# Optimization experiments

Hardware: AMD Instinct MI355X
Metric: run time of the kernel (lower is better)

Reference implementation:

```python
import jax, jax.numpy as jnp
import numpy as np

N = 16384        # nodes
E = 262144       # edges (avg degree 16)
MUL = 64         # multiplicity per irrep
RDIM = 8         # radial embedding dim
NEURONS = 64     # radial MLP hidden width
NSPECIES = 4
AVG_NEIGH = 16.0
SQRT3 = 1.7320508075688772


def setup_inputs() -> dict:
    key = jax.random.key(0)
    k = jax.random.split(key, 16)
    ey1 = jax.random.normal(k[3], (E, 3), jnp.float32)
    ey1 = ey1 / jnp.linalg.norm(ey1, axis=-1, keepdims=True)  # l=1 spherical harmonics ~ unit edge vectors
    return {
        'node_x0': jax.random.normal(k[0], (N, MUL), jnp.float32),
        'node_x1': jax.random.normal(k[1], (N, MUL, 3), jnp.float32),
        'edge_y0': jnp.ones((E,), jnp.float32),            # l=0 SH is constant
        'edge_y1': ey1,
        'radial_embedding': jax.random.uniform(k[4], (E, RDIM), jnp.float32),
        'senders': jax.random.randint(k[5], (E,), 0, N, dtype=jnp.int32),
        'receivers': jax.random.randint(k[6], (E,), 0, N, dtype=jnp.int32),
        'node_species': jax.random.randint(k[7], (N,), 0, NSPECIES, dtype=jnp.int32),
        'Wup0': jax.random.normal(k[8], (MUL, MUL), jnp.float32),
        'Wup1': jax.random.normal(k[9], (MUL, MUL), jnp.float32),
        'Rw1': jax.random.normal(k[10], (RDIM, NEURONS), jnp.float32),
        'Rw2': jax.random.normal(k[11], (NEURONS, 4 * MUL), jnp.float32),
        'Wd0': jax.random.normal(k[12], (2 * MUL, 2 * MUL), jnp.float32),
        'Wd1': jax.random.normal(k[13], (2 * MUL, MUL), jnp.float32),
        'Wsc0': jax.random.normal(k[14], (NSPECIES, MUL, 2 * MUL), jnp.float32),
        'Wsc1': jax.random.normal(k[15], (NSPECIES, MUL, MUL), jnp.float32),
    }


def reference(node_x0, node_x1, edge_y0, edge_y1, radial_embedding,
              senders, receivers, node_species,
              Wup0, Wup1, Rw1, Rw2, Wd0, Wd1, Wsc0, Wsc1):
    inv = 1.0 / jnp.sqrt(jnp.float32(MUL))
    # ---- linear_up: per-irrep channel mixing --------------------------------
    h0 = (node_x0 @ Wup0) * inv                              # [N, MUL] 0e
    h1 = jnp.einsum('nmc,mk->nkc', node_x1, Wup1) * inv      # [N, MUL, 3] 1o
    # ---- radial MLP -> per-edge tensor-product path weights -----------------
    hid = jax.nn.silu((radial_embedding @ Rw1) / jnp.sqrt(jnp.float32(RDIM)))
    w = ((hid @ Rw2) / jnp.sqrt(jnp.float32(NEURONS))).reshape(E, 4, MUL)
    # ---- gather sender features ---------------------------------------------
    s0 = h0[senders]                                         # [E, MUL]
    s1 = h1[senders]                                         # [E, MUL, 3]
    # ---- CG tensor product (lmax=1) with radial weights ----------------------
    m0a = w[:, 0] * s0 * edge_y0[:, None]                    # 0e x 0e -> 0e
    m0b = w[:, 1] * jnp.einsum('emc,ec->em', s1, edge_y1) / SQRT3  # 1o . 1o -> 0e
    m1a = w[:, 2][:, :, None] * s0[:, :, None] * edge_y1[:, None, :]  # 0e x 1o -> 1o
    m1b = w[:, 3][:, :, None] * s1 * edge_y0[:, None, None]          # 1o x 0e -> 1o
    # ---- scatter-sum to receivers, normalize by sqrt(avg_num_neighbours) ----
    denom = jnp.sqrt(jnp.float32(AVG_NEIGH))
    a0 = jax.ops.segment_sum(jnp.concatenate([m0a, m0b], axis=-1), receivers, num_segments=N) / denom  # [N, 2*MUL]
    a1 = jax.ops.segment_sum(jnp.concatenate([m1a, m1b], axis=1), receivers, num_segments=N) / denom   # [N, 2*MUL, 3]
    # ---- linear_down to gate irreps (MUL scalars + MUL gates, MUL vectors) ---
    inv2 = 1.0 / jnp.sqrt(jnp.float32(2 * MUL))
    d0 = (a0 @ Wd0) * inv2                                   # [N, 2*MUL]
    d1 = jnp.einsum('nmc,mk->nkc', a1, Wd1) * inv2           # [N, MUL, 3]
    # ---- species-indexed self connection (gather weights by species) --------
    all0 = jnp.einsum('nm,smk->nsk', node_x0, Wsc0) * inv    # [N, S, 2*MUL]
    sc0 = jnp.take_along_axis(all0, node_species[:, None, None], axis=1)[:, 0]
    all1 = jnp.einsum('nmc,smk->nskc', node_x1, Wsc1) * inv  # [N, S, MUL, 3]
    sc1 = jnp.take_along_axis(all1, node_species[:, None, None, None], axis=1)[:, 0]
    f0 = 0.5 * (d0 + sc0)
    f1 = 0.5 * (d1 + sc1)
    # ---- equivariant gate: even_act on scalars, even_gate_act on gates ------
    scalars = jax.nn.silu(f0[:, :MUL])                       # [N, MUL]
    gates = jax.nn.silu(f0[:, MUL:])                         # [N, MUL]
    vectors = f1 * gates[:, :, None]                         # [N, MUL, 3]
    return scalars, vectors
```

## Files before the change

kernel.cpp:

```cpp
#include <hip/hip_runtime.h>

#define NN 16384
#define NE 262144
#define N64 (NN * 64)

typedef unsigned short u16;
typedef __attribute__((ext_vector_type(8))) short short8;
typedef __attribute__((ext_vector_type(4))) float f32x4;

__device__ __forceinline__ float us2f(u16 u) {
    union { unsigned int i; float f; } v; v.i = ((unsigned int)u) << 16; return v.f;
}
__device__ __forceinline__ u16 f2us(float x) {
    union { float f; unsigned int i; } u; u.f = x;
    unsigned int r = u.i + 0x7FFF + ((u.i >> 16) & 1);
    return (u16)(r >> 16);
}
__device__ __forceinline__ float silu_f(float x) { return x / (1.0f + __expf(-x)); }
__device__ __forceinline__ float ldf(const void* p, long i, int f) {
    return f ? ((const float*)p)[i] : us2f(((const u16*)p)[i]);
}
__device__ __forceinline__ short8 f32x8_to_bf16(const float* p) {
    f32x4 a = *reinterpret_cast<const f32x4*>(p);
    f32x4 b = *reinterpret_cast<const f32x4*>(p + 4);
    short8 r;
    r[0] = (short)f2us(a[0]); r[1] = (short)f2us(a[1]);
    r[2] = (short)f2us(a[2]); r[3] = (short)f2us(a[3]);
    r[4] = (short)f2us(b[0]); r[5] = (short)f2us(b[1]);
    r[6] = (short)f2us(b[2]); r[7] = (short)f2us(b[3]);
    return r;
}

__global__ void k_sniff(const u16* __restrict__ re, int* __restrict__ flag) {
    int t = threadIdx.x;
    int hit = (re[t] >= 0x4000) ? 1 : 0;
    unsigned long long b = __ballot(hit);
    if (t == 0) *flag = (__popcll(b) >= 4) ? 1 : 0;
}

#define SB0 1048576L
#define SB1 4194304L
#define SB2 4456448L
#define SB3 5242880L
#define SB4 7340032L
#define SB5 7344128L
#define SB6 7348224L
#define SB7 7348736L
#define SB8 7365120L
#define SB9 7381504L
#define SB10 7389696L
#define SB11 7422464L
#define SB12 7438848L

__global__ void k_convert(const void* x0, const void* x1, const void* ey0, const void* ey1,
                          const void* re, const void* Wup0, const void* Wup1, const void* Rw1,
                          const void* Rw2, const void* Wd0, const void* Wd1, const void* Wsc0,
                          const void* Wsc1, const int* __restrict__ flag,
                          const int* __restrict__ recv, int* __restrict__ cnt,
                          u16* c_x0, u16* x1T, u16* c_ey0, u16* c_ey1, u16* c_re,
                          u16* c_Wup0, u16* c_Wup1, u16* c_Rw1, u16* c_Rw2,
                          u16* c_Wd0, u16* c_Wd1, u16* c_Wsc0, u16* c_Wsc1) {
    long i = (long)blockIdx.x * 256 + threadIdx.x;
    int f = *flag;
    if (i < NE) atomicAdd(&cnt[recv[i]], 1);
    if (i < SB0)       { c_x0[i]          = f2us(ldf(x0, i, f)); }
    else if (i < SB1)  {
        long j = i - SB0;
        int n = (int)(j / 192); int r = (int)(j % 192); int m = r / 3; int c = r % 3;
        x1T[(long)c * N64 + (long)n * 64 + m] = f2us(ldf(x1, j, f));
    }
    else if (i < SB2)  { c_ey0[i - SB1]   = f2us(ldf(ey0, i - SB1, f)); }
    else if (i < SB3)  { c_ey1[i - SB2]   = f2us(ldf(ey1, i - SB2, f)); }
    else if (i < SB4)  { c_re[i - SB3]    = f2us(ldf(re, i - SB3, f)); }
    else if (i < SB5)  { long j = i - SB4;  long r = j >> 6, c = j & 63;
                         c_Wup0[c * 64 + r]  = f2us(ldf(Wup0, j, f)); }
    else if (i < SB6)  { long j = i - SB5;  long r = j >> 6, c = j & 63;
                         c_Wup1[c * 64 + r]  = f2us(ldf(Wup1, j, f)); }
    else if (i < SB7)  { c_Rw1[i - SB6]   = f2us(ldf(Rw1, i - SB6, f)); }
    else if (i < SB8)  { long j = i - SB7;  long r = j >> 8, c = j & 255;
                         c_Rw2[c * 64 + r]   = f2us(ldf(Rw2, j, f)); }
    else if (i < SB9)  { long j = i - SB8;  long r = j >> 7, c = j & 127;
                         c_Wd0[c * 128 + r]  = f2us(ldf(Wd0, j, f)); }
    else if (i < SB10) { long j = i - SB9;  long r = j >> 6, c = j & 63;
                         c_Wd1[c * 128 + r]  = f2us(ldf(Wd1, j, f)); }
    else if (i < SB11) { long j = i - SB10; long s = j >> 13, rm = j & 8191;
                         long r = rm >> 7, c = rm & 127;
                         c_Wsc0[s * 8192 + c * 64 + r] = f2us(ldf(Wsc0, j, f)); }
    else               { long j = i - SB11; long s = j >> 12, rm = j & 4095;
                         long r = rm >> 6, c = rm & 63;
                         c_Wsc1[s * 4096 + c * 64 + r] = f2us(ldf(Wsc1, j, f)); }
}

__global__ void k_scan(const int* __restrict__ cnt, int* __restrict__ offs,
                       int* __restrict__ cursor) {
    __shared__ int sd[256];
    int t = threadIdx.x;
    int base = t * 64;
    const int4* c4 = (const int4*)cnt;
    int loc[64];
#pragma unroll
    for (int i = 0; i < 16; i++) {
        int4 v = c4[t * 16 + i];
        loc[i * 4 + 0] = v.x; loc[i * 4 + 1] = v.y; loc[i * 4 + 2] = v.z; loc[i * 4 + 3] = v.w;
    }
    int sum = 0;
#pragma unroll
    for (int i = 0; i < 64; i++) sum += loc[i];
    sd[t] = sum; __syncthreads();
    for (int off = 1; off < 256; off <<= 1) {
        int v = (t >= off) ? sd[t - off] : 0;
        __syncthreads();
        sd[t] += v;
        __syncthreads();
    }
    int run = sd[t] - sum;
    for (int i = 0; i < 64; i++) {
        offs[base + i] = run; cursor[base + i] = run;
        run += loc[i];
    }
    if (t == 255) offs[NN] = run;
}

__global__ void k_scatter(const int* __restrict__ recv, const int* __restrict__ senders,
                          const u16* __restrict__ ey0, const u16* __restrict__ ey1,
                          int* __restrict__ cursor, int4* __restrict__ meta) {
    int e = blockIdx.x * 256 + threadIdx.x;
    int node = recv[e];
    int p = atomicAdd(&cursor[node], 1);
    unsigned y0  = ey0[e];
    unsigned y1x = ey1[(long)e * 3 + 0];
    unsigned y1y = ey1[(long)e * 3 + 1];
    unsigned y1z = ey1[(long)e * 3 + 2];
    int4 m;
    m.x = senders[e];
    m.y = (int)(y0 | (y1x << 16));
    m.z = (int)(y1y | (y1z << 16));
    m.w = (int)((unsigned)e | ((unsigned)node << 18));
    meta[p] = m;
}

__global__ void k_up_gemm(const u16* __restrict__ x0, const u16* __restrict__ x1T,
                          const u16* __restrict__ Wup0, const u16* __restrict__ Wup1,
                          u16* __restrict__ h) {
    int inst = blockIdx.y;
    int wv = threadIdx.x >> 6, lane = threadIdx.x & 63;
    int lhi = lane >> 4, llo = lane & 15;
    int mb = blockIdx.x * 256 + wv * 64;
    const u16* B = (inst == 0) ? Wup0 : Wup1;
    const u16* A = (inst == 0) ? x0 : (x1T + (long)(inst - 1) * N64);

    short8 bfr[4][2];
#pragma unroll
    for (int t = 0; t < 4; t++)
#pragma unroll
        for (int s = 0; s < 2; s++)
            bfr[t][s] = *reinterpret_cast<const short8*>(B + (long)(t * 16 + llo) * 64 + s * 32 + lhi * 8);

    f32x4 acc[4][4];
#pragma unroll
    for (int i = 0; i < 4; i++)
#pragma unroll
        for (int t = 0; t < 4; t++) acc[i][t] = 0.0f;

#pragma unroll
    for (int s = 0; s < 2; s++) {
        short8 af[4];
#pragma unroll
        for (int i = 0; i < 4; i++)
            af[i] = *reinterpret_cast<const short8*>(A + (long)(mb + i * 16 + llo) * 64 + s * 32 + lhi * 8);
#pragma unroll
        for (int i = 0; i < 4; i++)
#pragma unroll
            for (int t = 0; t < 4; t++)
                acc[i][t] = __builtin_amdgcn_mfma_f32_16x16x32_bf16(af[i], bfr[t][s], acc[i][t], 0, 0, 0);
    }
#pragma unroll
    for (int i = 0; i < 4; i++)
#pragma unroll
        for (int t = 0; t < 4; t++)
#pragma unroll
            for (int r = 0; r < 4; r++)
                h[(long)(mb + i * 16 + lhi * 4 + r) * 256 + (t * 16 + llo) * 4 + inst] =
                    f2us(acc[i][t][r] * 0.125f);
}

#define RROW 276
__global__ void __launch_bounds__(256, 3)
k_edge(const u16* __restrict__ re, const u16* __restrict__ Rw1,
       const u16* __restrict__ Rw2, const int4* __restrict__ meta,
       const u16* __restrict__ h, float* __restrict__ abuf32) {
    __shared__ u16 hid_s[64][72];
    __shared__ u16 w_lds[64 * RROW];
    int tid = threadIdx.x;
    int wv = tid >> 6, lane = tid & 63, lhi = lane >> 4, llo = lane & 15;
    int p0 = blockIdx.x * 64;

    {
        int el = tid >> 2;
        int jb = (tid & 3) * 16;
        int e = ((const int*)meta)[(long)(p0 + el) * 4 + 3] & 0x3FFFF;
        short8 r8 = *reinterpret_cast<const short8*>(re + (long)e * 8);
        float rr[8];
#pragma unroll
        for (int r = 0; r < 8; r++) rr[r] = us2f((u16)r8[r]);
        float hv[16];
#pragma unroll
        for (int q = 0; q < 2; q++) {
            short8 w8 = *reinterpret_cast<const short8*>(Rw1 + jb + q * 8);
#pragma unroll
            for (int j = 0; j < 8; j++) hv[q * 8 + j] = rr[0] * us2f((u16)w8[j]);
        }
#pragma unroll
        for (int r = 1; r < 8; r++) {
#pragma unroll
            for (int q = 0; q < 2; q++) {
                short8 w8 = *reinterpret_cast<const short8*>(Rw1 + (long)r * 64 + jb + q * 8);
#pragma unroll
                for (int j = 0; j < 8; j++) hv[q * 8 + j] += rr[r] * us2f((u16)w8[j]);
            }
        }
#pragma unroll
        for (int q = 0; q < 4; q++) {
            ushort4 pk;
            pk.x = f2us(silu_f(hv[q * 4 + 0] * 0.35355339059327373f));
            pk.y = f2us(silu_f(hv[q * 4 + 1] * 0.35355339059327373f));
            pk.z = f2us(silu_f(hv[q * 4 + 2] * 0.35355339059327373f));
            pk.w = f2us(silu_f(hv[q * 4 + 3] * 0.35355339059327373f));
            *reinterpret_cast<ushort4*>(&hid_s[el][jb + q * 4]) = pk;
        }
    }
    __syncthreads();

    {
        short8 bfr[4][2];
#pragma unroll
        for (int t = 0; t < 4; t++)
#pragma unroll
            for (int s = 0; s < 2; s++)
                bfr[t][s] = *reinterpret_cast<const short8*>(
                    Rw2 + (long)(wv * 64 + t * 16 + llo) * 64 + s * 32 + lhi * 8);
        f32x4 acc[4][4];
#pragma unroll
        for (int i = 0; i < 4; i++)
#pragma unroll
            for (int t = 0; t < 4; t++) acc[i][t] = 0.0f;
#pragma unroll
        for (int s = 0; s < 2; s++) {
            short8 af[4];
#pragma unroll
            for (int i = 0; i < 4; i++)
                af[i] = *reinterpret_cast<const short8*>(&hid_s[i * 16 + llo][s * 32 + lhi * 8]);
#pragma unroll
            for (int i = 0; i < 4; i++)
#pragma unroll
                for (int t = 0; t < 4; t++)
                    acc[i][t] = __builtin_amdgcn_mfma_f32_16x16x32_bf16(af[i], bfr[t][s], acc[i][t], 0, 0, 0);
        }
#pragma unroll
        for (int i = 0; i < 4; i++)
#pragma unroll
            for (int t = 0; t < 4; t++)
#pragma unroll
                for (int r = 0; r < 4; r++)
                    w_lds[(i * 16 + lhi * 4 + r) * RROW + wv * 64 + t * 16 + llo] =
                        f2us(acc[i][t][r] * 0.125f);
    }
    __syncthreads();

    {
        const float qn = 0.25f;
        const float rs3 = 0.57735026918962576f;
        int l = lane;
        int base = wv * 16;
        float acc[8];
#pragma unroll
        for (int r = 0; r < 8; r++) acc[r] = 0.f;
        int cur = -1;

        int4 m = meta[p0 + base];
        ushort4 hv = *reinterpret_cast<const ushort4*>(h + (long)m.x * 256 + l * 4);

        for (int ss = 0; ss < 16; ss++) {
            int4 mn = m; ushort4 hn = hv;
            if (ss + 1 < 16) {
                mn = meta[p0 + base + ss + 1];
                hn = *reinterpret_cast<const ushort4*>(h + (long)mn.x * 256 + l * 4);
            }
            int node = (int)(((unsigned)m.w) >> 18);
            if (node != cur) {
                if (cur >= 0) {
                    float* dst = abuf32 + (long)cur * 512 + l;
                    atomicAdd(dst,        acc[0] * qn);
                    atomicAdd(dst + 64,   acc[1] * qn * rs3);
                    atomicAdd(dst + 128,  acc[2] * qn);
                    atomicAdd(dst + 192,  acc[3] * qn);
                    atomicAdd(dst + 256,  acc[4] * qn);
                    atomicAdd(dst + 320,  acc[5] * qn);
                    atomicAdd(dst + 384,  acc[6] * qn);
                    atomicAdd(dst + 448,  acc[7] * qn);
                }
                cur = node;
#pragma unroll
                for (int r = 0; r < 8; r++) acc[r] = 0.f;
            }
            int sl = base + ss;
            float w0 = us2f(w_lds[sl * RROW + l]);
            float w1 = us2f(w_lds[sl * RROW + 64 + l]);
            float w2 = us2f(w_lds[sl * RROW + 128 + l]);
            float w3 = us2f(w_lds[sl * RROW + 192 + l]);
            float y0  = us2f((u16)((unsigned)m.y & 0xffff));
            float y1x = us2f((u16)((unsigned)m.y >> 16));
            float y1y = us2f((u16)((unsigned)m.z & 0xffff));
            float y1z = us2f((u16)((unsigned)m.z >> 16));
            float s0 = us2f(hv.x), s1x = us2f(hv.y), s1y = us2f(hv.z), s1z = us2f(hv.w);
            acc[0] += w0 * s0 * y0;
            acc[1] += w1 * (s1x * y1x + s1y * y1y + s1z * y1z);
            acc[2] += w2 * s0 * y1x;  acc[3] += w3 * s1x * y0;
            acc[4] += w2 * s0 * y1y;  acc[5] += w3 * s1y * y0;
            acc[6] += w2 * s0 * y1z;  acc[7] += w3 * s1z * y0;
            m = mn; hv = hn;
        }
        {
            float* dst = abuf32 + (long)cur * 512 + l;
            atomicAdd(dst,        acc[0] * qn);
            atomicAdd(dst + 64,   acc[1] * qn * rs3);
            atomicAdd(dst + 128,  acc[2] * qn);
            atomicAdd(dst + 192,  acc[3] * qn);
            atomicAdd(dst + 256,  acc[4] * qn);
            atomicAdd(dst + 320,  acc[5] * qn);
            atomicAdd(dst + 384,  acc[6] * qn);
            atomicAdd(dst + 448,  acc[7] * qn);
        }
    }
}

#define DN 32
__global__ void __launch_bounds__(320, 3)
k_down(const float* __restrict__ abuf32, const u16* __restrict__ x0,
       const u16* __restrict__ x1T, const int* __restrict__ species,
       const u16* __restrict__ Wd0T, const u16* __restrict__ Wd1T,
       const u16* __restrict__ Wsc0T, const u16* __restrict__ Wsc1T,
       float* __restrict__ out) {
    __shared__ float gate_s[DN][65];
    __shared__ float vec_s[DN * 192];
    __shared__ int sp_s[DN];
    int tid = threadIdx.x;
    int g = tid >> 6;
    int lane = tid & 63, lhi = lane >> 4, llo = lane & 15;
    int node0 = blockIdx.x * DN;
    if (tid < DN) sp_s[tid] = species[node0 + tid];
    __syncthreads();

    const float* Ad; const u16* BdT; int bcol;
    const u16* As; const u16* BsT; int sstr;
    if (g <= 1) { Ad = abuf32; BdT = Wd0T; bcol = g * 64; As = x0; BsT = Wsc0T; sstr = 8192; }
    else        { Ad = abuf32 + (g - 1) * 128; BdT = Wd1T; bcol = 0;
                  As = x1T + (long)(g - 2) * N64; BsT = Wsc1T; sstr = 4096; }

    const float inv2 = 0.08838834764831845f;
    const float inv  = 0.125f;

    short8 a2[DN / 16][2];
#pragma unroll
    for (int rt = 0; rt < DN / 16; rt++)
#pragma unroll
        for (int ks = 0; ks < 2; ks++)
            a2[rt][ks] = *reinterpret_cast<const short8*>(
                As + (long)(node0 + rt * 16 + llo) * 64 + ks * 32 + lhi * 8);

    f32x4 res[DN / 16][4];
#pragma unroll
    for (int rt = 0; rt < DN / 16; rt++)
#pragma unroll
        for (int ct = 0; ct < 4; ct++) res[rt][ct] = 0.0f;

    for (int s = 0; s < 4; s++) {
        short8 bs[4][2];
#pragma unroll
        for (int ct = 0; ct < 4; ct++)
#pragma unroll
            for (int ks = 0; ks < 2; ks++)
                bs[ct][ks] = *reinterpret_cast<const short8*>(
                    BsT + (long)s * sstr + (long)(bcol + ct * 16 + llo) * 64 + ks * 32 + lhi * 8);
#pragma unroll
        for (int rt = 0; rt < DN / 16; rt++) {
            f32x4 accs[4];
#pragma unroll
            for (int ct = 0; ct < 4; ct++) accs[ct] = 0.0f;
#pragma unroll
            for (int ks = 0; ks < 2; ks++)
#pragma unroll
                for (int ct = 0; ct < 4; ct++)
                    accs[ct] = __builtin_amdgcn_mfma_f32_16x16x32_bf16(a2[rt][ks], bs[ct][ks], accs[ct], 0, 0, 0);
#pragma unroll
            for (int r = 0; r < 4; r++) {
                int sp = sp_s[rt * 16 + lhi * 4 + r];
                if (sp == s)
#pragma unroll
                    for (int ct = 0; ct < 4; ct++) res[rt][ct][r] = accs[ct][r];
            }
        }
    }

    short8 bd[4][4];
#pragma unroll
    for (int ct = 0; ct < 4; ct++)
#pragma unroll
        for (int ks = 0; ks < 4; ks++)
            bd[ct][ks] = *reinterpret_cast<const short8*>(
                BdT + (long)(bcol + ct * 16 + llo) * 128 + ks * 32 + lhi * 8);

#pragma unroll
    for (int rt = 0; rt < DN / 16; rt++) {
        f32x4 accd[4];
#pragma unroll
        for (int ct = 0; ct < 4; ct++) accd[ct] = 0.0f;
#pragma unroll
        for (int ks = 0; ks < 4; ks++) {
            short8 a = f32x8_to_bf16(Ad + (long)(node0 + rt * 16 + llo) * 512 + ks * 32 + lhi * 8);
#pragma unroll
            for (int ct = 0; ct < 4; ct++)
                accd[ct] = __builtin_amdgcn_mfma_f32_16x16x32_bf16(a, bd[ct][ks], accd[ct], 0, 0, 0);
        }
#pragma unroll
        for (int ct = 0; ct < 4; ct++)
#pragma unroll
            for (int r = 0; r < 4; r++) {
                float fvv = 0.5f * (accd[ct][r] * inv2 + res[rt][ct][r] * inv);
                int row = rt * 16 + lhi * 4 + r;
                int col = ct * 16 + llo;
                if (g == 0) {
                    out[(long)(node0 + row) * 64 + col] = silu_f(fvv);
                } else if (g == 1) {
                    gate_s[row][col] = silu_f(fvv);
                } else {
                    vec_s[row * 192 + col * 3 + (g - 2)] = fvv;
                }
            }
    }
    __syncthreads();

    {
        float* vout = out + (long)N64 + (long)node0 * 192;
        for (int q4 = tid; q4 < DN * 48; q4 += 320) {
            int q = q4 * 4;
            int row = q4 / 48;
            int rem = q - row * 192;
            f32x4 v = *reinterpret_cast<const f32x4*>(&vec_s[q]);
#pragma unroll
            for (int e = 0; e < 4; e++) v[e] *= gate_s[row][(rem + e) / 3];
            *reinterpret_cast<f32x4*>(vout + q) = v;
        }
    }
}

extern "C" void kernel_launch(void* const* d_in, const int* in_sizes, int n_in,
                              void* d_out, int out_size, void* d_ws, size_t ws_size,
                              hipStream_t stream) {
    const int* senders   = (const int*)d_in[5];
    const int* receivers = (const int*)d_in[6];
    const int* species   = (const int*)d_in[7];
    float* out = (float*)d_out;

    char* ws = (char*)d_ws;
    size_t o = 0;
    auto alloc = [&](size_t bytes) { size_t p = o; o = (o + bytes + 255) & ~255UL; return p; };
    int* flag   = (int*)(ws + alloc(4));
    int* cnt    = (int*)(ws + alloc((size_t)NN * 4));
    int* offs   = (int*)(ws + alloc((size_t)(NN + 1) * 4));
    int* cursor = (int*)(ws + alloc((size_t)NN * 4));
    int4* meta  = (int4*)(ws + alloc((size_t)NE * 16));
    u16* c_x0   = (u16*)(ws + alloc(SB0 * 2));
    u16* x1T    = (u16*)(ws + alloc((size_t)3 * N64 * 2));
    u16* c_ey0  = (u16*)(ws + alloc((SB2 - SB1) * 2));
    u16* c_ey1  = (u16*)(ws + alloc((SB3 - SB2) * 2));
    u16* c_re   = (u16*)(ws + alloc((SB4 - SB3) * 2));
    u16* c_Wup0 = (u16*)(ws + alloc((SB5 - SB4) * 2));
    u16* c_Wup1 = (u16*)(ws + alloc((SB6 - SB5) * 2));
    u16* c_Rw1  = (u16*)(ws + alloc((SB7 - SB6) * 2));
    u16* c_Rw2  = (u16*)(ws + alloc((SB8 - SB7) * 2));
    u16* c_Wd0  = (u16*)(ws + alloc((SB9 - SB8) * 2));
    u16* c_Wd1  = (u16*)(ws + alloc((SB10 - SB9) * 2));
    u16* c_Wsc0 = (u16*)(ws + alloc((SB11 - SB10) * 2));
    u16* c_Wsc1 = (u16*)(ws + alloc((SB12 - SB11) * 2));
    u16* h      = (u16*)(ws + alloc((size_t)NN * 256 * 2));
    float* abuf32 = (float*)(ws + alloc((size_t)NN * 512 * 4));

    k_sniff<<<1, 64, 0, stream>>>((const u16*)d_in[4], flag);
    (void)hipMemsetAsync(cnt, 0, (size_t)NN * 4, stream);
    (void)hipMemsetAsync(abuf32, 0, (size_t)NN * 512 * 4, stream);
    k_convert<<<29058, 256, 0, stream>>>(d_in[0], d_in[1], d_in[2], d_in[3], d_in[4],
        d_in[8], d_in[9], d_in[10], d_in[11], d_in[12], d_in[13], d_in[14], d_in[15],
        flag, receivers, cnt,
        c_x0, x1T, c_ey0, c_ey1, c_re,
        c_Wup0, c_Wup1, c_Rw1, c_Rw2, c_Wd0, c_Wd1, c_Wsc0, c_Wsc1);
    k_scan<<<1, 256, 0, stream>>>(cnt, offs, cursor);
    k_scatter<<<NE / 256, 256, 0, stream>>>(receivers, senders, c_ey0, c_ey1,
                                            cursor, meta);

    k_up_gemm<<<dim3(NN / 256, 4), 256, 0, stream>>>(c_x0, x1T, c_Wup0, c_Wup1, h);

    k_edge<<<NE / 64, 256, 0, stream>>>(c_re, c_Rw1, c_Rw2, meta, h, abuf32);

    k_down<<<NN / DN, 320, 0, stream>>>(abuf32, c_x0, x1T, species,
                                        c_Wd0, c_Wd1, c_Wsc0, c_Wsc1, out);
}
```

Baseline: 276.1 us.

## Replace global atomics with plain stores and LDS merge for receiver segments in edge kernel

Using the CSR offsets, the edge kernel now writes node aggregates with plain stores when a receiver's whole edge segment lies inside one wave's slice of the block. Segments that span waves inside the block are merged in LDS with shared atomics, then written once. Only segments crossing block boundaries still use global atomics. The hidden-activation scratch is aliased into the weight LDS buffer, with an added barrier, and occupancy is raised from 3 to 4 blocks per CU. In exchange it adds extra offset loads and branching per flush.

```diff
diff --git a/kernel.cpp b/kernel.cpp
--- a/kernel.cpp
+++ b/kernel.cpp
@@ -184,16 +184,24 @@
                     f2us(acc[i][t][r] * 0.125f);
 }
 
-#define RROW 276
-__global__ void __launch_bounds__(256, 3)
+#define RROW 268
+__global__ void __launch_bounds__(256, 4)
 k_edge(const u16* __restrict__ re, const u16* __restrict__ Rw1,
        const u16* __restrict__ Rw2, const int4* __restrict__ meta,
-       const u16* __restrict__ h, float* __restrict__ abuf32) {
-    __shared__ u16 hid_s[64][72];
+       const u16* __restrict__ h, const int* __restrict__ offs,
+       float* __restrict__ abuf32) {
     __shared__ u16 w_lds[64 * RROW];
+    __shared__ float mrg[3][512];
+    __shared__ int mrg_node[3], mrg_used[3], mrg_cont[3];
+    u16 (*hid_s)[72] = reinterpret_cast<u16 (*)[72]>(w_lds);
+
     int tid = threadIdx.x;
     int wv = tid >> 6, lane = tid & 63, lhi = lane >> 4, llo = lane & 15;
     int p0 = blockIdx.x * 64;
+
+#pragma unroll
+    for (int k = tid; k < 3 * 512; k += 256) (&mrg[0][0])[k] = 0.f;
+    if (tid < 3) mrg_used[tid] = 0;
 
     {
         int el = tid >> 2;
@@ -256,6 +264,7 @@
                 for (int t = 0; t < 4; t++)
                     acc[i][t] = __builtin_amdgcn_mfma_f32_16x16x32_bf16(af[i], bfr[t][s], acc[i][t], 0, 0, 0);
         }
+        __syncthreads();
 #pragma unroll
         for (int i = 0; i < 4; i++)
 #pragma unroll
@@ -271,39 +280,63 @@
         const float qn = 0.25f;
         const float rs3 = 0.57735026918962576f;
         int l = lane;
-        int base = wv * 16;
+        int wb = wv * 16;
         float acc[8];
 #pragma unroll
         for (int r = 0; r < 8; r++) acc[r] = 0.f;
         int cur = -1;
 
-        int4 m = meta[p0 + base];
+        int4 m = meta[p0 + wb];
         ushort4 hv = *reinterpret_cast<const ushort4*>(h + (long)m.x * 256 + l * 4);
+
+        auto flush = [&](int n) {
+            int s = offs[n], e = offs[n + 1];
+            int sb = s < p0 ? p0 : s;
+            int se = e > p0 + 64 ? p0 + 64 : e;
+            int w0 = (sb - p0) >> 4, w1 = (se - 1 - p0) >> 4;
+            float v0 = acc[0] * qn, v1 = acc[1] * qn * rs3;
+            float v2 = acc[2] * qn, v3 = acc[3] * qn;
+            float v4 = acc[4] * qn, v5 = acc[5] * qn;
+            float v6 = acc[6] * qn, v7 = acc[7] * qn;
+            if (w0 == w1) {
+                float* dst = abuf32 + (long)n * 512 + l;
+                if (s >= p0 && e <= p0 + 64) {
+                    dst[0]   = v0; dst[64]  = v1; dst[128] = v2; dst[192] = v3;
+                    dst[256] = v4; dst[320] = v5; dst[384] = v6; dst[448] = v7;
+                } else {
+                    atomicAdd(dst,       v0); atomicAdd(dst + 64,  v1);
+                    atomicAdd(dst + 128, v2); atomicAdd(dst + 192, v3);
+                    atomicAdd(dst + 256, v4); atomicAdd(dst + 320, v5);
+                    atomicAdd(dst + 384, v6); atomicAdd(dst + 448, v7);
+                }
+            } else {
+                int j = w0;
+                if (l == 0) {
+                    mrg_node[j] = n; mrg_used[j] = 1;
+                    mrg_cont[j] = (s >= p0 && e <= p0 + 64) ? 1 : 0;
+                }
+                float* md = &mrg[j][l];
+                atomicAdd(md,       v0); atomicAdd(md + 64,  v1);
+                atomicAdd(md + 128, v2); atomicAdd(md + 192, v3);
+                atomicAdd(md + 256, v4); atomicAdd(md + 320, v5);
+                atomicAdd(md + 384, v6); atomicAdd(md + 448, v7);
+            }
+        };
 
         for (int ss = 0; ss < 16; ss++) {
             int4 mn = m; ushort4 hn = hv;
             if (ss + 1 < 16) {
-                mn = meta[p0 + base + ss + 1];
+                mn = meta[p0 + wb + ss + 1];
                 hn = *reinterpret_cast<const ushort4*>(h + (long)mn.x * 256 + l * 4);
             }
             int node = (int)(((unsigned)m.w) >> 18);
             if (node != cur) {
-                if (cur >= 0) {
-                    float* dst = abuf32 + (long)cur * 512 + l;
-                    atomicAdd(dst,        acc[0] * qn);
-                    atomicAdd(dst + 64,   acc[1] * qn * rs3);
-                    atomicAdd(dst + 128,  acc[2] * qn);
-                    atomicAdd(dst + 192,  acc[3] * qn);
-                    atomicAdd(dst + 256,  acc[4] * qn);
-                    atomicAdd(dst + 320,  acc[5] * qn);
-                    atomicAdd(dst + 384,  acc[6] * qn);
-                    atomicAdd(dst + 448,  acc[7] * qn);
-                }
+                if (cur >= 0) flush(cur);
                 cur = node;
 #pragma unroll
                 for (int r = 0; r < 8; r++) acc[r] = 0.f;
             }
-            int sl = base + ss;
+            int sl = wb + ss;
             float w0 = us2f(w_lds[sl * RROW + l]);
             float w1 = us2f(w_lds[sl * RROW + 64 + l]);
             float w2 = us2f(w_lds[sl * RROW + 128 + l]);
@@ -320,16 +353,21 @@
             acc[6] += w2 * s0 * y1z;  acc[7] += w3 * s1z * y0;
             m = mn; hv = hn;
         }
-        {
-            float* dst = abuf32 + (long)cur * 512 + l;
-            atomicAdd(dst,        acc[0] * qn);
-            atomicAdd(dst + 64,   acc[1] * qn * rs3);
-            atomicAdd(dst + 128,  acc[2] * qn);
-            atomicAdd(dst + 192,  acc[3] * qn);
-            atomicAdd(dst + 256,  acc[4] * qn);
-            atomicAdd(dst + 320,  acc[5] * qn);
-            atomicAdd(dst + 384,  acc[6] * qn);
-            atomicAdd(dst + 448,  acc[7] * qn);
+        flush(cur);
+    }
+    __syncthreads();
+
+#pragma unroll
+    for (int j = 0; j < 3; j++) {
+        if (mrg_used[j]) {
+            int n = mrg_node[j];
+            float* dst = abuf32 + (long)n * 512;
+            float a = mrg[j][tid], b = mrg[j][tid + 256];
+            if (mrg_cont[j]) {
+                dst[tid] = a; dst[tid + 256] = b;
+            } else {
+                atomicAdd(dst + tid, a); atomicAdd(dst + tid + 256, b);
+            }
         }
     }
 }
@@ -500,7 +538,7 @@
 
     k_up_gemm<<<dim3(NN / 256, 4), 256, 0, stream>>>(c_x0, x1T, c_Wup0, c_Wup1, h);
 
-    k_edge<<<NE / 64, 256, 0, stream>>>(c_re, c_Rw1, c_Rw2, meta, h, abuf32);
+    k_edge<<<NE / 64, 256, 0, stream>>>(c_re, c_Rw1, c_Rw2, meta, h, offs, abuf32);
 
     k_down<<<NN / DN, 320, 0, stream>>>(abuf32, c_x0, x1T, species,
                                         c_Wd0, c_Wd1, c_Wsc0, c_Wsc1, out);
```

New measurement: 315.2 us. +14.2%, slower.

## Assign receiver-node ranges to edge blocks, replacing float atomics with bf16 stores

Applied to the files above, without the earlier changes.

The edge kernel now gives each block 16 consecutive receiver nodes and walks their CSR-sorted edge range in 64-edge tiles. Each wave owns whole nodes and writes the aggregated result once with plain stores instead of float atomicAdds. The aggregation buffer shrinks from fp32 to bf16 and no longer needs a memset, and the down kernel reads bf16 directly without converting. The risks are load imbalance from variable node degree, a sequential per-node loop with lower parallelism, and reads of meta past the last edge, which the extra 64-entry padding covers.

```diff
diff --git a/kernel.cpp b/kernel.cpp
--- a/kernel.cpp
+++ b/kernel.cpp
@@ -19,16 +19,6 @@
 __device__ __forceinline__ float silu_f(float x) { return x / (1.0f + __expf(-x)); }
 __device__ __forceinline__ float ldf(const void* p, long i, int f) {
     return f ? ((const float*)p)[i] : us2f(((const u16*)p)[i]);
-}
-__device__ __forceinline__ short8 f32x8_to_bf16(const float* p) {
-    f32x4 a = *reinterpret_cast<const f32x4*>(p);
-    f32x4 b = *reinterpret_cast<const f32x4*>(p + 4);
-    short8 r;
-    r[0] = (short)f2us(a[0]); r[1] = (short)f2us(a[1]);
-    r[2] = (short)f2us(a[2]); r[3] = (short)f2us(a[3]);
-    r[4] = (short)f2us(b[0]); r[5] = (short)f2us(b[1]);
-    r[6] = (short)f2us(b[2]); r[7] = (short)f2us(b[3]);
-    return r;
 }
 
 __global__ void k_sniff(const u16* __restrict__ re, int* __restrict__ flag) {
@@ -184,159 +174,169 @@
                     f2us(acc[i][t][r] * 0.125f);
 }
 
+#define EN 16
 #define RROW 276
 __global__ void __launch_bounds__(256, 3)
 k_edge(const u16* __restrict__ re, const u16* __restrict__ Rw1,
        const u16* __restrict__ Rw2, const int4* __restrict__ meta,
-       const u16* __restrict__ h, float* __restrict__ abuf32) {
+       const u16* __restrict__ h, const int* __restrict__ offs,
+       u16* __restrict__ abuf) {
     __shared__ u16 hid_s[64][72];
     __shared__ u16 w_lds[64 * RROW];
+    __shared__ int offs_s[EN + 1];
     int tid = threadIdx.x;
     int wv = tid >> 6, lane = tid & 63, lhi = lane >> 4, llo = lane & 15;
-    int p0 = blockIdx.x * 64;
-
-    {
-        int el = tid >> 2;
-        int jb = (tid & 3) * 16;
-        int e = ((const int*)meta)[(long)(p0 + el) * 4 + 3] & 0x3FFFF;
-        short8 r8 = *reinterpret_cast<const short8*>(re + (long)e * 8);
-        float rr[8];
-#pragma unroll
-        for (int r = 0; r < 8; r++) rr[r] = us2f((u16)r8[r]);
-        float hv[16];
-#pragma unroll
-        for (int q = 0; q < 2; q++) {
-            short8 w8 = *reinterpret_cast<const short8*>(Rw1 + jb + q * 8);
-#pragma unroll
-            for (int j = 0; j < 8; j++) hv[q * 8 + j] = rr[0] * us2f((u16)w8[j]);
+    int n0 = blockIdx.x * EN;
+    if (tid <= EN) offs_s[tid] = offs[n0 + tid];
+    __syncthreads();
+    int s0 = offs_s[0], s1 = offs_s[EN];
+    int T = (s1 - s0 + 63) >> 6;
+
+    const float qn = 0.25f;
+    const float rs3 = 0.57735026918962576f;
+    int ni = wv;
+    float acc[8];
+#pragma unroll
+    for (int r = 0; r < 8; r++) acc[r] = 0.f;
+
+    for (int t = 0; t < T; t++) {
+        int ts = s0 + t * 64;
+        {
+            int el = tid >> 2;
+            int jb = (tid & 3) * 16;
+            int e = ((const int*)meta)[(long)(ts + el) * 4 + 3] & 0x3FFFF;
+            short8 r8 = *reinterpret_cast<const short8*>(re + (long)e * 8);
+            float rr[8];
+#pragma unroll
+            for (int r = 0; r < 8; r++) rr[r] = us2f((u16)r8[r]);
+            float hv[16];
+#pragma unroll
+            for (int q = 0; q < 2; q++) {
+                short8 w8 = *reinterpret_cast<const short8*>(Rw1 + jb + q * 8);
+#pragma unroll
+                for (int j = 0; j < 8; j++) hv[q * 8 + j] = rr[0] * us2f((u16)w8[j]);
+            }
+#pragma unroll
+            for (int r = 1; r < 8; r++) {
+#pragma unroll
+                for (int q = 0; q < 2; q++) {
+                    short8 w8 = *reinterpret_cast<const short8*>(Rw1 + (long)r * 64 + jb + q * 8);
+#pragma unroll
+                    for (int j = 0; j < 8; j++) hv[q * 8 + j] += rr[r] * us2f((u16)w8[j]);
+                }
+            }
+#pragma unroll
+            for (int q = 0; q < 4; q++) {
+                ushort4 pk;
+                pk.x = f2us(silu_f(hv[q * 4 + 0] * 0.35355339059327373f));
+                pk.y = f2us(silu_f(hv[q * 4 + 1] * 0.35355339059327373f));
+                pk.z = f2us(silu_f(hv[q * 4 + 2] * 0.35355339059327373f));
+                pk.w = f2us(silu_f(hv[q * 4 + 3] * 0.35355339059327373f));
+                *reinterpret_cast<ushort4*>(&hid_s[el][jb + q * 4]) = pk;
+            }
         }
-#pragma unroll
-        for (int r = 1; r < 8; r++) {
-#pragma unroll
-            for (int q = 0; q < 2; q++) {
-                short8 w8 = *reinterpret_cast<const short8*>(Rw1 + (long)r * 64 + jb + q * 8);
-#pragma unroll
-                for (int j = 0; j < 8; j++) hv[q * 8 + j] += rr[r] * us2f((u16)w8[j]);
-            }
+        __syncthreads();
+
+        {
+            short8 bfr[4][2];
+#pragma unroll
+            for (int tt = 0; tt < 4; tt++)
+#pragma unroll
+                for (int s = 0; s < 2; s++)
+                    bfr[tt][s] = *reinterpret_cast<const short8*>(
+                        Rw2 + (long)(wv * 64 + tt * 16 + llo) * 64 + s * 32 + lhi * 8);
+            f32x4 ac[4][4];
+#pragma unroll
+            for (int i = 0; i < 4; i++)
+#pragma unroll
+                for (int tt = 0; tt < 4; tt++) ac[i][tt] = 0.0f;
+#pragma unroll
+            for (int s = 0; s < 2; s++) {
+                short8 af[4];
+#pragma unroll
+                for (int i = 0; i < 4; i++)
+                    af[i] = *reinterpret_cast<const short8*>(&hid_s[i * 16 + llo][s * 32 + lhi * 8]);
+#pragma unroll
+                for (int i = 0; i < 4; i++)
+#pragma unroll
+                    for (int tt = 0; tt < 4; tt++)
+                        ac[i][tt] = __builtin_amdgcn_mfma_f32_16x16x32_bf16(af[i], bfr[tt][s], ac[i][tt], 0, 0, 0);
+            }
+#pragma unroll
+            for (int i = 0; i < 4; i++)
+#pragma unroll
+                for (int tt = 0; tt < 4; tt++)
+#pragma unroll
+                    for (int r = 0; r < 4; r++)
+                        w_lds[(i * 16 + lhi * 4 + r) * RROW + wv * 64 + tt * 16 + llo] =
+                            f2us(ac[i][tt][r] * 0.125f);
         }
-#pragma unroll
-        for (int q = 0; q < 4; q++) {
-            ushort4 pk;
-            pk.x = f2us(silu_f(hv[q * 4 + 0] * 0.35355339059327373f));
-            pk.y = f2us(silu_f(hv[q * 4 + 1] * 0.35355339059327373f));
-            pk.z = f2us(silu_f(hv[q * 4 + 2] * 0.35355339059327373f));
-            pk.w = f2us(silu_f(hv[q * 4 + 3] * 0.35355339059327373f));
-            *reinterpret_cast<ushort4*>(&hid_s[el][jb + q * 4]) = pk;
+        __syncthreads();
+
+        {
+            int te = ts + 64;
+            while (ni < EN) {
+                int rs = offs_s[ni], ren = offs_s[ni + 1];
+                if (rs >= te) break;
+                int a = rs > ts ? rs : ts;
+                int b = ren < te ? ren : te;
+                if (a < b) {
+                    int4 m = meta[a];
+                    ushort4 hv = *reinterpret_cast<const ushort4*>(h + (long)m.x * 256 + lane * 4);
+                    for (int p = a; p < b; p++) {
+                        int4 mn = m; ushort4 hn = hv;
+                        if (p + 1 < b) {
+                            mn = meta[p + 1];
+                            hn = *reinterpret_cast<const ushort4*>(h + (long)mn.x * 256 + lane * 4);
+                        }
+                        int sl = p - ts;
+                        float w0 = us2f(w_lds[sl * RROW + lane]);
+                        float w1 = us2f(w_lds[sl * RROW + 64 + lane]);
+                        float w2 = us2f(w_lds[sl * RROW + 128 + lane]);
+                        float w3 = us2f(w_lds[sl * RROW + 192 + lane]);
+                        float y0  = us2f((u16)((unsigned)m.y & 0xffff));
+                        float y1x = us2f((u16)((unsigned)m.y >> 16));
+                        float y1y = us2f((u16)((unsigned)m.z & 0xffff));
+                        float y1z = us2f((u16)((unsigned)m.z >> 16));
+                        float sv0 = us2f(hv.x), s1x = us2f(hv.y), s1y = us2f(hv.z), s1z = us2f(hv.w);
+                        acc[0] += w0 * sv0 * y0;
+                        acc[1] += w1 * (s1x * y1x + s1y * y1y + s1z * y1z);
+                        acc[2] += w2 * sv0 * y1x;  acc[3] += w3 * s1x * y0;
+                        acc[4] += w2 * sv0 * y1y;  acc[5] += w3 * s1y * y0;
+                        acc[6] += w2 * sv0 * y1z;  acc[7] += w3 * s1z * y0;
+                        m = mn; hv = hn;
+                    }
+                }
+                if (ren <= te) {
+                    u16* ab = abuf + (long)(n0 + ni) * 512 + lane;
+                    ab[0]   = f2us(acc[0] * qn);
+                    ab[64]  = f2us(acc[1] * qn * rs3);
+                    ab[128] = f2us(acc[2] * qn);
+                    ab[192] = f2us(acc[3] * qn);
+                    ab[256] = f2us(acc[4] * qn);
+                    ab[320] = f2us(acc[5] * qn);
+                    ab[384] = f2us(acc[6] * qn);
+                    ab[448] = f2us(acc[7] * qn);
+#pragma unroll
+                    for (int r = 0; r < 8; r++) acc[r] = 0.f;
+                    ni += 4;
+                } else break;
+            }
         }
-    }
-    __syncthreads();
-
-    {
-        short8 bfr[4][2];
-#pragma unroll
-        for (int t = 0; t < 4; t++)
-#pragma unroll
-            for (int s = 0; s < 2; s++)
-                bfr[t][s] = *reinterpret_cast<const short8*>(
-                    Rw2 + (long)(wv * 64 + t * 16 + llo) * 64 + s * 32 + lhi * 8);
-        f32x4 acc[4][4];
-#pragma unroll
-        for (int i = 0; i < 4; i++)
-#pragma unroll
-            for (int t = 0; t < 4; t++) acc[i][t] = 0.0f;
-#pragma unroll
-        for (int s = 0; s < 2; s++) {
-            short8 af[4];
-#pragma unroll
-            for (int i = 0; i < 4; i++)
-                af[i] = *reinterpret_cast<const short8*>(&hid_s[i * 16 + llo][s * 32 + lhi * 8]);
-#pragma unroll
-            for (int i = 0; i < 4; i++)
-#pragma unroll
-                for (int t = 0; t < 4; t++)
-                    acc[i][t] = __builtin_amdgcn_mfma_f32_16x16x32_bf16(af[i], bfr[t][s], acc[i][t], 0, 0, 0);
-        }
-#pragma unroll
-        for (int i = 0; i < 4; i++)
-#pragma unroll
-            for (int t = 0; t < 4; t++)
-#pragma unroll
-                for (int r = 0; r < 4; r++)
-                    w_lds[(i * 16 + lhi * 4 + r) * RROW + wv * 64 + t * 16 + llo] =
-                        f2us(acc[i][t][r] * 0.125f);
-    }
-    __syncthreads();
-
-    {
-        const float qn = 0.25f;
-        const float rs3 = 0.57735026918962576f;
-        int l = lane;
-        int base = wv * 16;
-        float acc[8];
-#pragma unroll
-        for (int r = 0; r < 8; r++) acc[r] = 0.f;
-        int cur = -1;
-
-        int4 m = meta[p0 + base];
-        ushort4 hv = *reinterpret_cast<const ushort4*>(h + (long)m.x * 256 + l * 4);
-
-        for (int ss = 0; ss < 16; ss++) {
-            int4 mn = m; ushort4 hn = hv;
-            if (ss + 1 < 16) {
-                mn = meta[p0 + base + ss + 1];
-                hn = *reinterpret_cast<const ushort4*>(h + (long)mn.x * 256 + l * 4);
-            }
-            int node = (int)(((unsigned)m.w) >> 18);
-            if (node != cur) {
-                if (cur >= 0) {
-                    float* dst = abuf32 + (long)cur * 512 + l;
-                    atomicAdd(dst,        acc[0] * qn);
-                    atomicAdd(dst + 64,   acc[1] * qn * rs3);
-                    atomicAdd(dst + 128,  acc[2] * qn);
-                    atomicAdd(dst + 192,  acc[3] * qn);
-                    atomicAdd(dst + 256,  acc[4] * qn);
-                    atomicAdd(dst + 320,  acc[5] * qn);
-                    atomicAdd(dst + 384,  acc[6] * qn);
-                    atomicAdd(dst + 448,  acc[7] * qn);
-                }
-                cur = node;
-#pragma unroll
-                for (int r = 0; r < 8; r++) acc[r] = 0.f;
-            }
-            int sl = base + ss;
-            float w0 = us2f(w_lds[sl * RROW + l]);
-            float w1 = us2f(w_lds[sl * RROW + 64 + l]);
-            float w2 = us2f(w_lds[sl * RROW + 128 + l]);
-            float w3 = us2f(w_lds[sl * RROW + 192 + l]);
-            float y0  = us2f((u16)((unsigned)m.y & 0xffff));
-            float y1x = us2f((u16)((unsigned)m.y >> 16));
-            float y1y = us2f((u16)((unsigned)m.z & 0xffff));
-            float y1z = us2f((u16)((unsigned)m.z >> 16));
-            float s0 = us2f(hv.x), s1x = us2f(hv.y), s1y = us2f(hv.z), s1z = us2f(hv.w);
-            acc[0] += w0 * s0 * y0;
-            acc[1] += w1 * (s1x * y1x + s1y * y1y + s1z * y1z);
-            acc[2] += w2 * s0 * y1x;  acc[3] += w3 * s1x * y0;
-            acc[4] += w2 * s0 * y1y;  acc[5] += w3 * s1y * y0;
-            acc[6] += w2 * s0 * y1z;  acc[7] += w3 * s1z * y0;
-            m = mn; hv = hn;
-        }
-        {
-            float* dst = abuf32 + (long)cur * 512 + l;
-            atomicAdd(dst,        acc[0] * qn);
-            atomicAdd(dst + 64,   acc[1] * qn * rs3);
-            atomicAdd(dst + 128,  acc[2] * qn);
-            atomicAdd(dst + 192,  acc[3] * qn);
-            atomicAdd(dst + 256,  acc[4] * qn);
-            atomicAdd(dst + 320,  acc[5] * qn);
-            atomicAdd(dst + 384,  acc[6] * qn);
-            atomicAdd(dst + 448,  acc[7] * qn);
-        }
+        __syncthreads();
+    }
+    while (ni < EN) {
+        u16* ab = abuf + (long)(n0 + ni) * 512 + lane;
+        u16 z = f2us(0.f);
+        ab[0] = z; ab[64] = z; ab[128] = z; ab[192] = z;
+        ab[256] = z; ab[320] = z; ab[384] = z; ab[448] = z;
+        ni += 4;
     }
 }
 
 #define DN 32
 __global__ void __launch_bounds__(320, 3)
-k_down(const float* __restrict__ abuf32, const u16* __restrict__ x0,
+k_down(const u16* __restrict__ abuf, const u16* __restrict__ x0,
        const u16* __restrict__ x1T, const int* __restrict__ species,
        const u16* __restrict__ Wd0T, const u16* __restrict__ Wd1T,
        const u16* __restrict__ Wsc0T, const u16* __restrict__ Wsc1T,
@@ -351,10 +351,10 @@
     if (tid < DN) sp_s[tid] = species[node0 + tid];
     __syncthreads();
 
-    const float* Ad; const u16* BdT; int bcol;
+    const u16* Ad; const u16* BdT; int bcol;
     const u16* As; const u16* BsT; int sstr;
-    if (g <= 1) { Ad = abuf32; BdT = Wd0T; bcol = g * 64; As = x0; BsT = Wsc0T; sstr = 8192; }
-    else        { Ad = abuf32 + (g - 1) * 128; BdT = Wd1T; bcol = 0;
+    if (g <= 1) { Ad = abuf; BdT = Wd0T; bcol = g * 64; As = x0; BsT = Wsc0T; sstr = 8192; }
+    else        { Ad = abuf + (g - 1) * 128; BdT = Wd1T; bcol = 0;
                   As = x1T + (long)(g - 2) * N64; BsT = Wsc1T; sstr = 4096; }
 
     const float inv2 = 0.08838834764831845f;
@@ -417,7 +417,8 @@
         for (int ct = 0; ct < 4; ct++) accd[ct] = 0.0f;
 #pragma unroll
         for (int ks = 0; ks < 4; ks++) {
-            short8 a = f32x8_to_bf16(Ad + (long)(node0 + rt * 16 + llo) * 512 + ks * 32 + lhi * 8);
+            short8 a = *reinterpret_cast<const short8*>(
+                Ad + (long)(node0 + rt * 16 + llo) * 512 + ks * 32 + lhi * 8);
 #pragma unroll
             for (int ct = 0; ct < 4; ct++)
                 accd[ct] = __builtin_amdgcn_mfma_f32_16x16x32_bf16(a, bd[ct][ks], accd[ct], 0, 0, 0);
@@ -469,7 +470,7 @@
     int* cnt    = (int*)(ws + alloc((size_t)NN * 4));
     int* offs   = (int*)(ws + alloc((size_t)(NN + 1) * 4));
     int* cursor = (int*)(ws + alloc((size_t)NN * 4));
-    int4* meta  = (int4*)(ws + alloc((size_t)NE * 16));
+    int4* meta  = (int4*)(ws + alloc((size_t)(NE + 64) * 16));
     u16* c_x0   = (u16*)(ws + alloc(SB0 * 2));
     u16* x1T    = (u16*)(ws + alloc((size_t)3 * N64 * 2));
     u16* c_ey0  = (u16*)(ws + alloc((SB2 - SB1) * 2));
@@ -484,11 +485,10 @@
     u16* c_Wsc0 = (u16*)(ws + alloc((SB11 - SB10) * 2));
     u16* c_Wsc1 = (u16*)(ws + alloc((SB12 - SB11) * 2));
     u16* h      = (u16*)(ws + alloc((size_t)NN * 256 * 2));
-    float* abuf32 = (float*)(ws + alloc((size_t)NN * 512 * 4));
+    u16* abuf   = (u16*)(ws + alloc((size_t)NN * 512 * 2));
 
     k_sniff<<<1, 64, 0, stream>>>((const u16*)d_in[4], flag);
     (void)hipMemsetAsync(cnt, 0, (size_t)NN * 4, stream);
-    (void)hipMemsetAsync(abuf32, 0, (size_t)NN * 512 * 4, stream);
     k_convert<<<29058, 256, 0, stream>>>(d_in[0], d_in[1], d_in[2], d_in[3], d_in[4],
         d_in[8], d_in[9], d_in[10], d_in[11], d_in[12], d_in[13], d_in[14], d_in[15],
         flag, receivers, cnt,
@@ -500,8 +500,8 @@
 
     k_up_gemm<<<dim3(NN / 256, 4), 256, 0, stream>>>(c_x0, x1T, c_Wup0, c_Wup1, h);
 
-    k_edge<<<NE / 64, 256, 0, stream>>>(c_re, c_Rw1, c_Rw2, meta, h, abuf32);
-
-    k_down<<<NN / DN, 320, 0, stream>>>(abuf32, c_x0, x1T, species,
+    k_edge<<<NN / EN, 256, 0, stream>>>(c_re, c_Rw1, c_Rw2, meta, h, offs, abuf);
+
+    k_down<<<NN / DN, 320, 0, stream>>>(abuf, c_x0, x1T, species,
                                         c_Wd0, c_Wd1, c_Wsc0, c_Wsc1, out);
 }
```

New measurement: 427.9 us. 1.55x slower.
